# Kernel optimization log

Measured on AMD Instinct MI355X. Metric: run time of the kernel, lower is better.

## Reference

```python
import jax, jax.numpy as jnp
import numpy as np

H = 768      # hidden size
F = 3072     # FFN intermediate (4*H)
E = 8        # num experts
K = 2        # top_k
B, S = 2, 2048


def setup_inputs() -> dict:
    key = jax.random.key(0)
    ks = jax.random.split(key, 6)
    scale_in = 1.0 / np.sqrt(H)
    scale_mid = 1.0 / np.sqrt(F)
    return {
        "x": jax.random.normal(ks[0], (B, S, H), dtype=jnp.float32),
        "gate_w": jax.random.normal(ks[1], (H, E), dtype=jnp.float32) * scale_in,
        "W1": jax.random.normal(ks[2], (E, H, F), dtype=jnp.float32) * scale_in,
        "b1": jnp.zeros((E, F), dtype=jnp.float32),
        "W2": jax.random.normal(ks[3], (E, F, H), dtype=jnp.float32) * scale_mid,
        "b2": jnp.zeros((E, H), dtype=jnp.float32),
    }


def reference(x, gate_w, W1, b1, W2, b2):
    """MoE FFN: top-k router -> per-expert FFN -> weighted combine.

    Faithful to the torch module: router logits = x @ gate_w (no bias),
    softmax over the top-k logits only, each expert is a dense FFN
    (Linear -> GELU -> Linear), output = sum_k w_k * expert_{idx_k}(x).
    Expressed densely: combine weights are scattered into a [T, E] matrix
    (zero for unselected experts), so running every expert on every token
    and contracting with the combine matrix yields identical math.
    """
    batch, seq_len, hidden = x.shape
    xf = x.reshape(-1, hidden)                       # [T, H]
    T = xf.shape[0]

    logits = xf @ gate_w                             # [T, E]
    top_w, top_idx = jax.lax.top_k(logits, K)        # [T, K]
    top_w = jax.nn.softmax(top_w, axis=-1)

    # scatter top-k softmax weights into dense [T, E] combine matrix
    comb = jnp.zeros((T, E), dtype=x.dtype).at[
        jnp.arange(T)[:, None], top_idx
    ].add(top_w)

    # all experts on all tokens (zero combine weight kills unselected)
    h = jnp.einsum('th,ehf->etf', xf, W1) + b1[:, None, :]   # [E, T, F]
    h = jax.nn.gelu(h)
    y = jnp.einsum('etf,efh->eth', h, W2) + b2[:, None, :]   # [E, T, H]

    out = jnp.einsum('te,eth->th', comb, y)                  # [T, H]
    return out.reshape(batch, seq_len, hidden)
```

## Files before the change

kernel.cpp:

```cpp
#include <hip/hip_runtime.h>

#define H 768
#define F 3072
#define NE 8
#define T 4096
#define NA 8192
#define TP 9216
#define NRB 72

typedef unsigned short ushort_t;
typedef __attribute__((ext_vector_type(8))) short bfx8;
typedef __attribute__((ext_vector_type(4))) float fx4;
typedef __attribute__((address_space(3))) const ushort_t lus;

__device__ __forceinline__ ushort_t f2bf(float f) {
    union { float f; unsigned u; } v; v.f = f;
    unsigned u = v.u;
    unsigned r = (u + 0x7fffu + ((u >> 16) & 1u)) >> 16;
    return (ushort_t)r;
}

__device__ __forceinline__ float gelu_tanh(float x) {
    const float c = 0.7978845608028654f;
    float z = c * (x + 0.044715f * x * x * x);
    float t = 1.0f - 2.0f / (__expf(2.0f * z) + 1.0f);
    return 0.5f * x * (1.0f + t);
}

__device__ __forceinline__ void g2l16(const void* g, void* l) {
    __builtin_amdgcn_global_load_lds(
        (__attribute__((address_space(1))) void*)g,
        (__attribute__((address_space(3))) void*)l, 16, 0, 0);
}

__device__ __forceinline__ bfx8 dsr128(lus* p) {
    bfx8 r;
    asm volatile("ds_read_b128 %0, %1" : "=v"(r) : "v"(p));
    return r;
}

#define WAITV4 asm volatile("s_waitcnt vmcnt(4)" ::: "memory")
#define WAITV0 asm volatile("s_waitcnt vmcnt(0)" ::: "memory")
#define LGKM6  asm volatile("s_waitcnt lgkmcnt(6)" ::: "memory")
#define LGKM0  asm volatile("s_waitcnt lgkmcnt(0)" ::: "memory")
#define SBAR   asm volatile("s_barrier" ::: "memory")
#define SCHED0 __builtin_amdgcn_sched_barrier(0)
#define PRIO1  __builtin_amdgcn_s_setprio(1)
#define PRIO0  __builtin_amdgcn_s_setprio(0)

__global__ void router_k(const float* __restrict__ x, const float* __restrict__ gw,
                         int* __restrict__ tidx, float* __restrict__ twgt) {
    int t = blockIdx.x * 4 + (threadIdx.x >> 6);
    int lane = threadIdx.x & 63;
    const float* xr = x + (size_t)t * H;
    float acc[NE];
#pragma unroll
    for (int e = 0; e < NE; ++e) acc[e] = 0.f;
    for (int h = lane; h < H; h += 64) {
        float xv = xr[h];
        const float* g = gw + h * NE;
#pragma unroll
        for (int e = 0; e < NE; ++e) acc[e] += xv * g[e];
    }
#pragma unroll
    for (int off = 32; off > 0; off >>= 1) {
#pragma unroll
        for (int e = 0; e < NE; ++e) acc[e] += __shfl_down(acc[e], off);
    }
    if (lane == 0) {
        float l0 = -1e30f, l1 = -1e30f; int i0 = 0, i1 = 0;
#pragma unroll
        for (int e = 0; e < NE; ++e) {
            float v = acc[e];
            if (v > l0) { l1 = l0; i1 = i0; l0 = v; i0 = e; }
            else if (v > l1) { l1 = v; i1 = e; }
        }
        float w0 = 1.f / (1.f + __expf(l1 - l0));
        tidx[t * 2] = i0; tidx[t * 2 + 1] = i1;
        twgt[t * 2] = w0; twgt[t * 2 + 1] = 1.f - w0;
    }
}

__global__ void init_k(int* counts, int* tos) {
    int i = blockIdx.x * 256 + threadIdx.x;
    if (i < NE) counts[i] = 0;
    if (i < TP) tos[i] = -1;
}

__global__ void count_k(const int* __restrict__ tidx, int* counts) {
    int i = blockIdx.x * 256 + threadIdx.x;
    if (i < NA) atomicAdd(&counts[tidx[i]], 1);
}

__global__ void offsets_k(const int* __restrict__ counts, int* cursor,
                          int* rbe, int* rbs) {
    int off = 0, rb = 0;
    for (int e = 0; e < NE; ++e) {
        cursor[e] = off;
        int nrb = (counts[e] + 127) / 128;
        for (int j = 0; j < nrb; ++j) { rbe[rb] = e; rbs[rb] = off + j * 128; ++rb; }
        off += nrb * 128;
    }
    for (; rb < NRB; ++rb) rbe[rb] = -1;
}

__global__ void scatter_k(const int* __restrict__ tidx, int* cursor,
                          int* __restrict__ tos, int* __restrict__ aslot) {
    int i = blockIdx.x * 256 + threadIdx.x;
    if (i < NA) {
        int e = tidx[i];
        int slot = atomicAdd(&cursor[e], 1);
        tos[slot] = i >> 1;
        aslot[i] = slot;
    }
}

__global__ void gather_k(const float* __restrict__ x, const int* __restrict__ tos,
                         ushort_t* __restrict__ xg) {
    int i = blockIdx.x * 256 + threadIdx.x;
    int slot = i / (H / 8);
    int j = i % (H / 8);
    int tok = tos[slot];
    ushort_t v[8];
    if (tok < 0) {
#pragma unroll
        for (int q = 0; q < 8; ++q) v[q] = 0;
    } else {
        const float* src = x + (size_t)tok * H + j * 8;
#pragma unroll
        for (int q = 0; q < 8; ++q) v[q] = f2bf(src[q]);
    }
    *(bfx8*)&xg[(size_t)slot * H + j * 8] = *(const bfx8*)v;
}

__global__ void transpose_cast_k(const float* __restrict__ src, ushort_t* __restrict__ dst,
                                 int R, int C) {
    int e = blockIdx.z;
    src += (size_t)e * R * C;
    dst += (size_t)e * R * C;
    int c0 = blockIdx.x * 64, r0 = blockIdx.y * 64;
    __shared__ float tile[64][65];
    int tid = threadIdx.x;
    int cc = tid & 63, rr = tid >> 6;
#pragma unroll
    for (int rep = 0; rep < 16; ++rep) {
        int r = rep * 4 + rr;
        tile[r][cc] = src[(size_t)(r0 + r) * C + c0 + cc];
    }
    __syncthreads();
#pragma unroll
    for (int rep = 0; rep < 16; ++rep) {
        int c = rep * 4 + rr;
        dst[(size_t)(c0 + c) * R + r0 + cc] = f2bf(tile[cc][c]);
    }
}

template <int DO_GELU>
__global__ __launch_bounds__(512, 4)
void gemm_tile_k(const ushort_t* __restrict__ A, const ushort_t* __restrict__ Bt,
                 const float* __restrict__ bias, void* __restrict__ Cout,
                 const int* __restrict__ rbe, const int* __restrict__ rbs,
                 int K, int N, int ncb) {
    constexpr int BUFS = 16384;
    int nwg = gridDim.x, bid = blockIdx.x;
    int wgid = (bid & 7) * (nwg >> 3) + (bid >> 3);
    int rb = wgid / ncb, cb = wgid % ncb;
    int e = rbe[rb];
    if (e < 0) return;
    int slot0 = rbs[rb];

    __shared__ __align__(16) ushort_t lds[2 * BUFS];

    int tid = threadIdx.x, lane = tid & 63, wid = tid >> 6;
    int wm = wid >> 2, wn = wid & 3;
    int l15 = lane & 15, qh = lane >> 4, sw = l15 & 7;

    const ushort_t* Ab = A + (size_t)slot0 * K;
    const ushort_t* Bb = Bt + ((size_t)e * N + cb * 128) * K;

    int j = tid >> 3, q = tid & 7;
    int cs = (q ^ (j & 7)) * 8;
    int ldsw = wid * 512;
    const ushort_t* aSrc = Ab + (size_t)j * K + cs;
    const ushort_t* bSrc = Bb + (size_t)j * K + cs;

    int ch0 = (qh ^ sw) << 3;
    int ch1 = ((4 + qh) ^ sw) << 3;
    int abase = (wm * 64 + l15) * 64;
    int bbase = 8192 + (wn * 32 + l15) * 64;

#define STAGE_T(BUF, KT) do { \
    _Pragma("unroll") for (int u = 0; u < 2; ++u) \
        g2l16(aSrc + (size_t)u * 64 * K + (KT) * 64, \
              &lds[(BUF) * BUFS + u * 4096 + ldsw]); \
    _Pragma("unroll") for (int u = 0; u < 2; ++u) \
        g2l16(bSrc + (size_t)u * 64 * K + (KT) * 64, \
              &lds[(BUF) * BUFS + 8192 + u * 4096 + ldsw]); \
} while (0)

    fx4 acc[4][2];
#pragma unroll
    for (int m = 0; m < 4; ++m)
#pragma unroll
        for (int n = 0; n < 2; ++n) acc[m][n] = (fx4){0.f, 0.f, 0.f, 0.f};
    bfx8 a0[4], a1[4], b0v[2], b1v[2];

    int NT = K >> 6;
    STAGE_T(0, 0);
    STAGE_T(1, 1);

#define KBODY(BUF, TT) do { \
    if ((TT) + 1 < NT) { WAITV4; } else { WAITV0; } \
    SBAR; \
    { \
      int ab = (BUF) * BUFS + abase, bb = (BUF) * BUFS + bbase; \
      _Pragma("unroll") for (int m = 0; m < 4; ++m) a0[m] = dsr128((lus*)&lds[ab + m * 1024 + ch0]); \
      _Pragma("unroll") for (int n = 0; n < 2; ++n) b0v[n] = dsr128((lus*)&lds[bb + n * 1024 + ch0]); \
      _Pragma("unroll") for (int m = 0; m < 4; ++m) a1[m] = dsr128((lus*)&lds[ab + m * 1024 + ch1]); \
      _Pragma("unroll") for (int n = 0; n < 2; ++n) b1v[n] = dsr128((lus*)&lds[bb + n * 1024 + ch1]); \
    } \
    LGKM6; SCHED0; \
    PRIO1; \
    _Pragma("unroll") for (int m = 0; m < 4; ++m) \
    _Pragma("unroll") for (int n = 0; n < 2; ++n) \
        acc[m][n] = __builtin_amdgcn_mfma_f32_16x16x32_bf16(a0[m], b0v[n], acc[m][n], 0, 0, 0); \
    PRIO0; \
    LGKM0; SCHED0; \
    PRIO1; \
    _Pragma("unroll") for (int m = 0; m < 4; ++m) \
    _Pragma("unroll") for (int n = 0; n < 2; ++n) \
        acc[m][n] = __builtin_amdgcn_mfma_f32_16x16x32_bf16(a1[m], b1v[n], acc[m][n], 0, 0, 0); \
    PRIO0; \
    SBAR; \
    if ((TT) + 2 < NT) STAGE_T(BUF, (TT) + 2); \
} while (0)

    for (int t = 0; t < NT; t += 2) {
        KBODY(0, t);
        KBODY(1, t + 1);
    }
#undef KBODY
#undef STAGE_T

#pragma unroll
    for (int n = 0; n < 2; ++n) {
        int col = cb * 128 + wn * 32 + n * 16 + l15;
        float bvv = bias[(size_t)e * N + col];
#pragma unroll
        for (int m = 0; m < 4; ++m) {
            int rowb = slot0 + wm * 64 + m * 16 + qh * 4;
            fx4 v = acc[m][n];
#pragma unroll
            for (int jj = 0; jj < 4; ++jj) {
                float val = v[jj] + bvv;
                if (DO_GELU) {
                    ((ushort_t*)Cout)[(size_t)(rowb + jj) * N + col] = f2bf(gelu_tanh(val));
                } else {
                    ((float*)Cout)[(size_t)(rowb + jj) * N + col] = val;
                }
            }
        }
    }
}

__global__ void combine_k(const float* __restrict__ y, const int* __restrict__ aslot,
                          const float* __restrict__ twgt, float* __restrict__ out) {
    int i = blockIdx.x * 256 + threadIdx.x;
    int t = i / (H / 4);
    int j = i % (H / 4);
    int s0 = aslot[t * 2], s1 = aslot[t * 2 + 1];
    float w0 = twgt[t * 2], w1 = twgt[t * 2 + 1];
    const float4 a = ((const float4*)(y + (size_t)s0 * H))[j];
    const float4 b = ((const float4*)(y + (size_t)s1 * H))[j];
    float4 r;
    r.x = w0 * a.x + w1 * b.x;
    r.y = w0 * a.y + w1 * b.y;
    r.z = w0 * a.z + w1 * b.z;
    r.w = w0 * a.w + w1 * b.w;
    ((float4*)(out + (size_t)t * H))[j] = r;
}

extern "C" void kernel_launch(void* const* d_in, const int* in_sizes, int n_in,
                              void* d_out, int out_size, void* d_ws, size_t ws_size,
                              hipStream_t stream) {
    const float* x  = (const float*)d_in[0];
    const float* gw = (const float*)d_in[1];
    const float* W1 = (const float*)d_in[2];
    const float* b1 = (const float*)d_in[3];
    const float* W2 = (const float*)d_in[4];
    const float* b2 = (const float*)d_in[5];
    float* out = (float*)d_out;

    char* ws = (char*)d_ws;
    size_t o = 0;
    auto carve = [&](size_t bytes) -> void* {
        o = (o + 255) & ~(size_t)255;
        void* p = ws + o;
        o += bytes;
        return p;
    };
    int*      tidx   = (int*)carve((size_t)NA * 4);
    float*    twgt   = (float*)carve((size_t)NA * 4);
    int*      counts = (int*)carve(NE * 4);
    int*      cursor = (int*)carve(NE * 4);
    int*      rbe    = (int*)carve(NRB * 4);
    int*      rbs    = (int*)carve(NRB * 4);
    int*      aslot  = (int*)carve((size_t)NA * 4);
    int*      tos    = (int*)carve((size_t)TP * 4);
    ushort_t* xg     = (ushort_t*)carve((size_t)TP * H * 2);
    ushort_t* w1t    = (ushort_t*)carve((size_t)NE * H * F * 2);
    ushort_t* w2t    = (ushort_t*)carve((size_t)NE * H * F * 2);
    ushort_t* hbuf   = (ushort_t*)carve((size_t)TP * F * 2);
    float*    ybuf   = (float*)xg;
    (void)in_sizes; (void)n_in; (void)out_size; (void)ws_size;

    hipLaunchKernelGGL(init_k, dim3(TP / 256), dim3(256), 0, stream, counts, tos);
    hipLaunchKernelGGL(router_k, dim3(T / 4), dim3(256), 0, stream, x, gw, tidx, twgt);
    hipLaunchKernelGGL(count_k, dim3(NA / 256), dim3(256), 0, stream, tidx, counts);
    hipLaunchKernelGGL(offsets_k, dim3(1), dim3(1), 0, stream, counts, cursor, rbe, rbs);
    hipLaunchKernelGGL(scatter_k, dim3(NA / 256), dim3(256), 0, stream, tidx, cursor, tos, aslot);
    hipLaunchKernelGGL(gather_k, dim3(TP * (H / 8) / 256), dim3(256), 0, stream, x, tos, xg);
    hipLaunchKernelGGL(transpose_cast_k, dim3(F / 64, H / 64, NE), dim3(256), 0, stream, W1, w1t, H, F);
    hipLaunchKernelGGL(transpose_cast_k, dim3(H / 64, F / 64, NE), dim3(256), 0, stream, W2, w2t, F, H);
    hipLaunchKernelGGL((gemm_tile_k<1>), dim3(NRB * (F / 128)), dim3(512), 0, stream,
                       xg, w1t, b1, (void*)hbuf, rbe, rbs, H, F, F / 128);
    hipLaunchKernelGGL((gemm_tile_k<0>), dim3(NRB * (H / 128)), dim3(512), 0, stream,
                       hbuf, w2t, b2, (void*)ybuf, rbe, rbs, F, H, H / 128);
    hipLaunchKernelGGL(combine_k, dim3(T * (H / 4) / 256), dim3(256), 0, stream,
                       ybuf, aslot, twgt, out);
}
```

Baseline: 251.0 us.

## Replace double-buffered LDS pipeline with single buffer in expert GEMM

The GEMM kernel's two-stage LDS double buffer is replaced with a single 32KB buffer, and each K-tile load is now fully waited on before compute. This halves LDS use per workgroup, which could raise occupancy. In exchange, global-to-LDS loads no longer overlap with MFMA compute, exposing load latency on every iteration.

```diff
diff --git a/kernel.cpp b/kernel.cpp
--- a/kernel.cpp
+++ b/kernel.cpp
@@ -39,7 +39,6 @@
     return r;
 }
 
-#define WAITV4 asm volatile("s_waitcnt vmcnt(4)" ::: "memory")
 #define WAITV0 asm volatile("s_waitcnt vmcnt(0)" ::: "memory")
 #define LGKM6  asm volatile("s_waitcnt lgkmcnt(6)" ::: "memory")
 #define LGKM0  asm volatile("s_waitcnt lgkmcnt(0)" ::: "memory")
@@ -161,7 +160,6 @@
                  const float* __restrict__ bias, void* __restrict__ Cout,
                  const int* __restrict__ rbe, const int* __restrict__ rbs,
                  int K, int N, int ncb) {
-    constexpr int BUFS = 16384;
     int nwg = gridDim.x, bid = blockIdx.x;
     int wgid = (bid & 7) * (nwg >> 3) + (bid >> 3);
     int rb = wgid / ncb, cb = wgid % ncb;
@@ -169,7 +167,7 @@
     if (e < 0) return;
     int slot0 = rbs[rb];
 
-    __shared__ __align__(16) ushort_t lds[2 * BUFS];
+    __shared__ __align__(16) ushort_t lds[16384];
 
     int tid = threadIdx.x, lane = tid & 63, wid = tid >> 6;
     int wm = wid >> 2, wn = wid & 3;
@@ -189,13 +187,11 @@
     int abase = (wm * 64 + l15) * 64;
     int bbase = 8192 + (wn * 32 + l15) * 64;
 
-#define STAGE_T(BUF, KT) do { \
+#define STAGE_T(KT) do { \
     _Pragma("unroll") for (int u = 0; u < 2; ++u) \
-        g2l16(aSrc + (size_t)u * 64 * K + (KT) * 64, \
-              &lds[(BUF) * BUFS + u * 4096 + ldsw]); \
+        g2l16(aSrc + (size_t)u * 64 * K + (KT) * 64, &lds[u * 4096 + ldsw]); \
     _Pragma("unroll") for (int u = 0; u < 2; ++u) \
-        g2l16(bSrc + (size_t)u * 64 * K + (KT) * 64, \
-              &lds[(BUF) * BUFS + 8192 + u * 4096 + ldsw]); \
+        g2l16(bSrc + (size_t)u * 64 * K + (KT) * 64, &lds[8192 + u * 4096 + ldsw]); \
 } while (0)
 
     fx4 acc[4][2];
@@ -206,40 +202,38 @@
     bfx8 a0[4], a1[4], b0v[2], b1v[2];
 
     int NT = K >> 6;
-    STAGE_T(0, 0);
-    STAGE_T(1, 1);
-
-#define KBODY(BUF, TT) do { \
-    if ((TT) + 1 < NT) { WAITV4; } else { WAITV0; } \
-    SBAR; \
-    { \
-      int ab = (BUF) * BUFS + abase, bb = (BUF) * BUFS + bbase; \
-      _Pragma("unroll") for (int m = 0; m < 4; ++m) a0[m] = dsr128((lus*)&lds[ab + m * 1024 + ch0]); \
-      _Pragma("unroll") for (int n = 0; n < 2; ++n) b0v[n] = dsr128((lus*)&lds[bb + n * 1024 + ch0]); \
-      _Pragma("unroll") for (int m = 0; m < 4; ++m) a1[m] = dsr128((lus*)&lds[ab + m * 1024 + ch1]); \
-      _Pragma("unroll") for (int n = 0; n < 2; ++n) b1v[n] = dsr128((lus*)&lds[bb + n * 1024 + ch1]); \
-    } \
-    LGKM6; SCHED0; \
-    PRIO1; \
-    _Pragma("unroll") for (int m = 0; m < 4; ++m) \
-    _Pragma("unroll") for (int n = 0; n < 2; ++n) \
-        acc[m][n] = __builtin_amdgcn_mfma_f32_16x16x32_bf16(a0[m], b0v[n], acc[m][n], 0, 0, 0); \
-    PRIO0; \
-    LGKM0; SCHED0; \
-    PRIO1; \
-    _Pragma("unroll") for (int m = 0; m < 4; ++m) \
-    _Pragma("unroll") for (int n = 0; n < 2; ++n) \
-        acc[m][n] = __builtin_amdgcn_mfma_f32_16x16x32_bf16(a1[m], b1v[n], acc[m][n], 0, 0, 0); \
-    PRIO0; \
-    SBAR; \
-    if ((TT) + 2 < NT) STAGE_T(BUF, (TT) + 2); \
-} while (0)
-
-    for (int t = 0; t < NT; t += 2) {
-        KBODY(0, t);
-        KBODY(1, t + 1);
-    }
-#undef KBODY
+    STAGE_T(0);
+
+    for (int t = 0; t < NT; ++t) {
+        WAITV0;
+        SBAR;
+#pragma unroll
+        for (int m = 0; m < 4; ++m) a0[m] = dsr128((lus*)&lds[abase + m * 1024 + ch0]);
+#pragma unroll
+        for (int n = 0; n < 2; ++n) b0v[n] = dsr128((lus*)&lds[bbase + n * 1024 + ch0]);
+#pragma unroll
+        for (int m = 0; m < 4; ++m) a1[m] = dsr128((lus*)&lds[abase + m * 1024 + ch1]);
+#pragma unroll
+        for (int n = 0; n < 2; ++n) b1v[n] = dsr128((lus*)&lds[bbase + n * 1024 + ch1]);
+        LGKM6; SCHED0;
+        PRIO1;
+#pragma unroll
+        for (int m = 0; m < 4; ++m)
+#pragma unroll
+            for (int n = 0; n < 2; ++n)
+                acc[m][n] = __builtin_amdgcn_mfma_f32_16x16x32_bf16(a0[m], b0v[n], acc[m][n], 0, 0, 0);
+        PRIO0;
+        LGKM0; SCHED0;
+        PRIO1;
+#pragma unroll
+        for (int m = 0; m < 4; ++m)
+#pragma unroll
+            for (int n = 0; n < 2; ++n)
+                acc[m][n] = __builtin_amdgcn_mfma_f32_16x16x32_bf16(a1[m], b1v[n], acc[m][n], 0, 0, 0);
+        PRIO0;
+        SBAR;
+        if (t + 1 < NT) STAGE_T(t + 1);
+    }
 #undef STAGE_T
 
 #pragma unroll
```

Result: slower. 259.2 us (+3.3%).

## Fuse expert counting into router and vectorize weight transpose-cast

Applied to the files above, without the earlier changes.

Removes the separate count kernel by having the router's lane 0 atomically increment the per-expert counts. The init kernel is replaced with hipMemsetAsync calls. The weight transpose-cast kernel now loads float4 and writes 4-wide bf16 vectors instead of scalar accesses, which reduces memory instructions on the large W1/W2 conversion. Risks include LDS bank conflicts on the column reads in the transpose and memset call overhead.

```diff
diff --git a/kernel.cpp b/kernel.cpp
--- a/kernel.cpp
+++ b/kernel.cpp
@@ -10,6 +10,7 @@
 
 typedef unsigned short ushort_t;
 typedef __attribute__((ext_vector_type(8))) short bfx8;
+typedef __attribute__((ext_vector_type(4))) short sx4;
 typedef __attribute__((ext_vector_type(4))) float fx4;
 typedef __attribute__((address_space(3))) const ushort_t lus;
 
@@ -49,7 +50,8 @@
 #define PRIO0  __builtin_amdgcn_s_setprio(0)
 
 __global__ void router_k(const float* __restrict__ x, const float* __restrict__ gw,
-                         int* __restrict__ tidx, float* __restrict__ twgt) {
+                         int* __restrict__ tidx, float* __restrict__ twgt,
+                         int* __restrict__ counts) {
     int t = blockIdx.x * 4 + (threadIdx.x >> 6);
     int lane = threadIdx.x & 63;
     const float* xr = x + (size_t)t * H;
@@ -78,18 +80,9 @@
         float w0 = 1.f / (1.f + __expf(l1 - l0));
         tidx[t * 2] = i0; tidx[t * 2 + 1] = i1;
         twgt[t * 2] = w0; twgt[t * 2 + 1] = 1.f - w0;
-    }
-}
-
-__global__ void init_k(int* counts, int* tos) {
-    int i = blockIdx.x * 256 + threadIdx.x;
-    if (i < NE) counts[i] = 0;
-    if (i < TP) tos[i] = -1;
-}
-
-__global__ void count_k(const int* __restrict__ tidx, int* counts) {
-    int i = blockIdx.x * 256 + threadIdx.x;
-    if (i < NA) atomicAdd(&counts[tidx[i]], 1);
+        atomicAdd(&counts[i0], 1);
+        atomicAdd(&counts[i1], 1);
+    }
 }
 
 __global__ void offsets_k(const int* __restrict__ counts, int* cursor,
@@ -141,17 +134,23 @@
     int c0 = blockIdx.x * 64, r0 = blockIdx.y * 64;
     __shared__ float tile[64][65];
     int tid = threadIdx.x;
-    int cc = tid & 63, rr = tid >> 6;
-#pragma unroll
-    for (int rep = 0; rep < 16; ++rep) {
-        int r = rep * 4 + rr;
-        tile[r][cc] = src[(size_t)(r0 + r) * C + c0 + cc];
+    int lr = tid >> 4;
+    int lc = (tid & 15) * 4;
+#pragma unroll
+    for (int p = 0; p < 4; ++p) {
+        int r = p * 16 + lr;
+        float4 v = *(const float4*)&src[(size_t)(r0 + r) * C + c0 + lc];
+        tile[r][lc] = v.x; tile[r][lc + 1] = v.y;
+        tile[r][lc + 2] = v.z; tile[r][lc + 3] = v.w;
     }
     __syncthreads();
 #pragma unroll
-    for (int rep = 0; rep < 16; ++rep) {
-        int c = rep * 4 + rr;
-        dst[(size_t)(c0 + c) * R + r0 + cc] = f2bf(tile[cc][c]);
+    for (int p = 0; p < 4; ++p) {
+        int c = p * 16 + lr;
+        ushort_t o[4];
+#pragma unroll
+        for (int k2 = 0; k2 < 4; ++k2) o[k2] = f2bf(tile[lc + k2][c]);
+        *(sx4*)&dst[(size_t)(c0 + c) * R + r0 + lc] = *(const sx4*)o;
     }
 }
 
@@ -314,9 +313,9 @@
     float*    ybuf   = (float*)xg;
     (void)in_sizes; (void)n_in; (void)out_size; (void)ws_size;
 
-    hipLaunchKernelGGL(init_k, dim3(TP / 256), dim3(256), 0, stream, counts, tos);
-    hipLaunchKernelGGL(router_k, dim3(T / 4), dim3(256), 0, stream, x, gw, tidx, twgt);
-    hipLaunchKernelGGL(count_k, dim3(NA / 256), dim3(256), 0, stream, tidx, counts);
+    hipMemsetAsync(counts, 0, NE * 4, stream);
+    hipMemsetAsync(tos, 0xFF, (size_t)TP * 4, stream);
+    hipLaunchKernelGGL(router_k, dim3(T / 4), dim3(256), 0, stream, x, gw, tidx, twgt, counts);
     hipLaunchKernelGGL(offsets_k, dim3(1), dim3(1), 0, stream, counts, cursor, rbe, rbs);
     hipLaunchKernelGGL(scatter_k, dim3(NA / 256), dim3(256), 0, stream, tidx, cursor, tos, aslot);
     hipLaunchKernelGGL(gather_k, dim3(TP * (H / 8) / 256), dim3(256), 0, stream, x, tos, xg);
```

Result: slower. 314.3 us (+25.2%).
